# Optimization experiments

Measured on AMD Instinct MI355X. Metric: run time of the kernel, lower is better.

The kernel has to match this reference:

```python
import jax, jax.numpy as jnp
import numpy as np

N = 12  # mmse_block_size
REAL_SIZE = N * (N + 1) // 2  # 78: diag + strict lower
IMAG_SIZE = N * (N - 1) // 2  # 66: strict lower only
ROWS, COLS = jnp.tril_indices(N)        # row-major (i, j<=i) matches torch loop order
ROWS_S, COLS_S = jnp.tril_indices(N, -1)  # strict lower, row-major, matches imag loop
DIAG_MASK = jnp.eye(N, dtype=bool)


def _mlp(x, W1, b1, W2, b2, W3, b3):
    h = jax.nn.relu(x @ W1 + b1)
    h = jax.nn.relu(h @ W2 + b2)
    return h @ W3 + b3


def _cholesky_outer(flat):
    # flat: [B, REAL_SIZE + IMAG_SIZE] -> [B, N, N] complex, L @ L^H
    B = flat.shape[0]
    L_real = jnp.zeros((B, N, N), flat.dtype).at[:, ROWS, COLS].set(flat[:, :REAL_SIZE])
    L_real = jnp.where(DIAG_MASK, jax.nn.softplus(L_real), L_real)
    L_imag = jnp.zeros((B, N, N), flat.dtype).at[:, ROWS_S, COLS_S].set(
        flat[:, REAL_SIZE:REAL_SIZE + IMAG_SIZE])
    L = L_real + 1j * L_imag
    return jnp.einsum('bij,bkj->bik', L, jnp.conj(L))


def setup_inputs() -> dict:
    key = jax.random.key(0)
    ks = jax.random.split(key, 13)
    L, H, OUT = 4096, 64, REAL_SIZE + IMAG_SIZE
    sc = lambda k, shp, fan: (jax.random.normal(k, shp, jnp.float32) / np.sqrt(fan))
    return {
        'channel_stats': jax.random.normal(ks[0], (8192, L), jnp.float32),
        'WC1': sc(ks[1], (L, H), L), 'bC1': jnp.zeros((H,), jnp.float32),
        'WC2': sc(ks[2], (H, H), H), 'bC2': jnp.zeros((H,), jnp.float32),
        'WC3': sc(ks[3], (H, OUT), H), 'bC3': jnp.zeros((OUT,), jnp.float32),
        'WR1': sc(ks[4], (L, H), L), 'bR1': jnp.zeros((H,), jnp.float32),
        'WR2': sc(ks[5], (H, H), H), 'bR2': jnp.zeros((H,), jnp.float32),
        'WR3': sc(ks[6], (H, OUT), H), 'bR3': jnp.zeros((OUT,), jnp.float32),
    }


def reference(channel_stats, WC1, bC1, WC2, bC2, WC3, bC3,
              WR1, bR1, WR2, bR2, WR3, bR3):
    C_flat = _mlp(channel_stats, WC1, bC1, WC2, bC2, WC3, bC3)
    R_flat = _mlp(channel_stats, WR1, bR1, WR2, bR2, WR3, bR3)
    C = _cholesky_outer(C_flat)
    R = _cholesky_outer(R_flat)
    return C, R
```

## Files before the change

kernel.cpp:

```cpp
#include <hip/hip_runtime.h>
#include <stdint.h>

#define M_ROWS 8192
#define K_DIM  4096
#define OUTD   144
#define PLANE  1179648
#define NT     32

typedef __attribute__((ext_vector_type(4))) float  float4v;
typedef __attribute__((ext_vector_type(8))) short  short8v;

static __device__ __forceinline__ unsigned short f2bf(float f) {
    unsigned int u = __builtin_bit_cast(unsigned int, f);
    u += 0x7FFFu + ((u >> 16) & 1u);
    return (unsigned short)(u >> 16);
}

__global__ __launch_bounds__(256) void wt_kernel(
    const float* __restrict__ WC1, const float* __restrict__ WR1,
    unsigned short* __restrict__ Wt) {
    __shared__ float tile[64][65];
    const float* src = (blockIdx.y == 0) ? WC1 : WR1;
    const int k0 = blockIdx.x * 64;
    const int t = threadIdx.x;
    const int j = t & 63, qq = t >> 6;
#pragma unroll
    for (int p = 0; p < 16; ++p) {
        int i = p * 4 + qq;
        tile[i][j] = src[(size_t)(k0 + i) * 64 + j];
    }
    __syncthreads();
    const int tt  = blockIdx.x >> 1;
    const int ksb = (blockIdx.x & 1) * 2;
#pragma unroll
    for (int p = 0; p < 16; ++p) {
        int c = p * 256 + t;
        int e = c & 7, m = (c >> 3) & 15, q = (c >> 7) & 3;
        int ks_l = (c >> 9) & 1, w_l = (c >> 10) & 3;
        int kp = ks_l * 32 + q * 8 + e;
        int np = w_l * 16 + m;
        int wg = blockIdx.y * 4 + w_l;
        size_t dst = ((size_t)(wg * 32 + tt) * 4 + (ksb + ks_l)) * 512
                   + q * 128 + m * 8 + e;
        Wt[dst] = f2bf(tile[kp][np]);
    }
}


#define ISSUE_B(T_, B0_, B1_, B2_, B3_)                          \
    do { const unsigned short* bp_ = bpw + (size_t)(T_) * 2048;  \
         B0_ = *(const short8v*)(bp_ + 0 * 512);                 \
         B1_ = *(const short8v*)(bp_ + 1 * 512);                 \
         B2_ = *(const short8v*)(bp_ + 2 * 512);                 \
         B3_ = *(const short8v*)(bp_ + 3 * 512); } while (0)

#define ISSUE_A(T_, XL_, XH_)                                    \
    do { const float* ap_ = xpw + (size_t)(T_) * 128;            \
         XL_ = *(const float4*)(ap_);                            \
         XH_ = *(const float4*)(ap_ + 4); } while (0)

#define STORE_A(XL_, XH_, BUF_)                                        \
    do { short8v s_;                                                   \
         s_[0] = (short)f2bf((XL_).x); s_[1] = (short)f2bf((XL_).y);   \
         s_[2] = (short)f2bf((XL_).z); s_[3] = (short)f2bf((XL_).w);   \
         s_[4] = (short)f2bf((XH_).x); s_[5] = (short)f2bf((XH_).y);   \
         s_[6] = (short)f2bf((XH_).z); s_[7] = (short)f2bf((XH_).w);   \
         *(short8v*)(Asm_ + (BUF_) * 2048 + (w * 64 + lane) * 8) = s_; } while (0)

#define MFR(BUF_, B0_, B1_, B2_, B3_)                                          \
    do { const unsigned short* ab_ = Asm_ + (BUF_) * 2048 + lane * 8;          \
         short8v a0_ = *(const short8v*)(ab_ + 0 * 512);                       \
         short8v a1_ = *(const short8v*)(ab_ + 1 * 512);                       \
         short8v a2_ = *(const short8v*)(ab_ + 2 * 512);                       \
         short8v a3_ = *(const short8v*)(ab_ + 3 * 512);                       \
         acc = __builtin_amdgcn_mfma_f32_16x16x32_bf16(a0_, B0_, acc, 0, 0, 0);\
         acc = __builtin_amdgcn_mfma_f32_16x16x32_bf16(a1_, B1_, acc, 0, 0, 0);\
         acc = __builtin_amdgcn_mfma_f32_16x16x32_bf16(a2_, B2_, acc, 0, 0, 0);\
         acc = __builtin_amdgcn_mfma_f32_16x16x32_bf16(a3_, B3_, acc, 0, 0, 0);\
    } while (0)

__global__ __launch_bounds__(512, 4) void fused_kernel(
    const float* __restrict__ X, const unsigned short* __restrict__ Wt,
    const float* __restrict__ bC1, const float* __restrict__ bR1,
    const float* __restrict__ WC2, const float* __restrict__ bC2,
    const float* __restrict__ WR2, const float* __restrict__ bR2,
    const float* __restrict__ WC3, const float* __restrict__ bC3,
    const float* __restrict__ WR3, const float* __restrict__ bR3,
    unsigned short* __restrict__ OUT) {
    __shared__ __align__(16) char smem[41216];
    unsigned short* Asm_ = (unsigned short*)smem;
    float* hs  = (float*)smem;
    float* W2s = hs + 16 * 132;
    float* fl  = W2s;

    const int tid  = threadIdx.x;
    const int lane = tid & 63;
    const int w    = tid >> 6;
    const int r0   = blockIdx.x * 16;
    const int m    = lane & 15, q = lane >> 4;

    float4v acc = {0.f, 0.f, 0.f, 0.f};

    const unsigned short* bpw = Wt + (size_t)w * 32 * 2048 + lane * 8;
    const float* xpw = X + (size_t)(r0 + m) * K_DIM + w * 32 + q * 8;
    const bool stager = (w < 4);

    short8v b00, b01, b02, b03, b10, b11, b12, b13;
    float4 xl0, xh0, xl1, xh1;

    ISSUE_B(0, b00, b01, b02, b03);
    if (stager) ISSUE_A(0, xl0, xh0);

#pragma unroll 1
    for (int t = 0; t < NT; t += 2) {
        if (stager) { STORE_A(xl0, xh0, 0); ISSUE_A(t + 1, xl1, xh1); }
        asm volatile("s_waitcnt lgkmcnt(0)" ::: "memory");
        __builtin_amdgcn_s_barrier();
        __builtin_amdgcn_sched_barrier(0);
        ISSUE_B(t + 1, b10, b11, b12, b13);
        MFR(0, b00, b01, b02, b03);
        if (stager) {
            STORE_A(xl1, xh1, 1);
            if (t + 2 < NT) ISSUE_A(t + 2, xl0, xh0);
        }
        asm volatile("s_waitcnt lgkmcnt(0)" ::: "memory");
        __builtin_amdgcn_s_barrier();
        __builtin_amdgcn_sched_barrier(0);
        if (t + 2 < NT) ISSUE_B(t + 2, b00, b01, b02, b03);
        MFR(1, b10, b11, b12, b13);
    }
    __syncthreads();

    {
        const int c = w * 16 + m;
        const float bv = (c < 64) ? bC1[c] : bR1[c - 64];
#pragma unroll
        for (int i = 0; i < 4; ++i) {
            int r = q * 4 + i;
            float v = acc[i] + bv; v = v > 0.f ? v : 0.f;
            hs[r * 132 + c] = v;
        }
    }
#pragma unroll
    for (int p = 0; p < 4; ++p) {
        int fi = p * 512 + tid;
        int k = fi >> 5, c4 = fi & 31;
        int c = c4 * 4;
        const float* wsrc = (c < 64) ? (WC2 + (size_t)k * 64 + c)
                                     : (WR2 + (size_t)k * 64 + (c - 64));
        *(float4*)&W2s[k * 128 + c] = *(const float4*)wsrc;
    }
    __syncthreads();

    const int rg = tid >> 5;
    const int cg = tid & 31;
    const int koff2 = (cg < 16) ? 0 : 64;
    float acc2[4];
    {
        int c = cg * 4;
        const float* bsrc = (c < 64) ? (bC2 + c) : (bR2 + (c - 64));
#pragma unroll
        for (int j = 0; j < 4; ++j) acc2[j] = bsrc[j];
    }
    for (int k = 0; k < 64; ++k) {
        float4 wv = *(const float4*)&W2s[k * 128 + cg * 4];
        float a = hs[rg * 132 + koff2 + k];
        acc2[0] += a * wv.x; acc2[1] += a * wv.y;
        acc2[2] += a * wv.z; acc2[3] += a * wv.w;
    }
    float4 h2v;
    h2v.x = acc2[0] > 0.f ? acc2[0] : 0.f;
    h2v.y = acc2[1] > 0.f ? acc2[1] : 0.f;
    h2v.z = acc2[2] > 0.f ? acc2[2] : 0.f;
    h2v.w = acc2[3] > 0.f ? acc2[3] : 0.f;
    __syncthreads();
    *(float4*)&hs[rg * 132 + cg * 4] = h2v;
    __syncthreads();

#pragma unroll 1
    for (int pass = 0; pass < 3; ++pass) {
        int c = pass * 128 + cg * 4;
        if (c < 288) {
            const int brn = (c >= 144);
            const int cl = c - (brn ? 144 : 0);
            const float* W3 = brn ? WR3 : WC3;
            const float* b3 = brn ? bR3 : bC3;
            const int ko = brn ? 64 : 0;
            float a3[4];
#pragma unroll
            for (int j = 0; j < 4; ++j) a3[j] = b3[cl + j];
            for (int k = 0; k < 64; ++k) {
                float4 wv = *(const float4*)(W3 + (size_t)k * OUTD + cl);
                float a = hs[rg * 132 + ko + k];
                a3[0] += a * wv.x; a3[1] += a * wv.y;
                a3[2] += a * wv.z; a3[3] += a * wv.w;
            }
            float4 v; v.x = a3[0]; v.y = a3[1]; v.z = a3[2]; v.w = a3[3];
            *(float4*)&fl[rg * 288 + c] = v;
        }
    }
    __syncthreads();

    if (tid < 384) {
        int r = tid / 24, rem = tid % 24;
        int brn = rem / 12, ii = rem % 12;
        float* f = &fl[r * 288 + brn * 144];
        int d = ii * (ii + 1) / 2 + ii;
        float xv = f[d];
        f[d] = (xv > 20.f) ? xv : log1pf(expf(xv));
    }
    __syncthreads();

    unsigned int* O32 = (unsigned int*)OUT;
    for (int task = tid; task < 16 * 2 * 78; task += 512) {
        int r = task / 156, rem = task % 156;
        int brn = rem / 78, p = rem % 78;
        int i = 0;
        while (p >= (i + 1) * (i + 2) / 2) ++i;
        int j = p - i * (i + 1) / 2;
        const float* f = &fl[r * 288 + brn * 144];
        const float* g = f + 78;
        const int ti = i * (i + 1) / 2, tj = j * (j + 1) / 2;
        const int si = i * (i - 1) / 2, sj = j * (j - 1) / 2;
        float re = 0.f, im = 0.f;
        for (int k = 0; k <= j; ++k) {
            float ar_ = f[ti + k];
            float ai  = (k == i) ? 0.f : g[si + k];
            float br_ = f[tj + k];
            float bi  = (k == j) ? 0.f : g[sj + k];
            re += ar_ * br_ + ai * bi;
            im += ai * br_ - ar_ * bi;
        }
        unsigned int reb = (unsigned int)f2bf(re);
        unsigned int imb = (unsigned int)f2bf(im);
        unsigned int imn = (unsigned int)f2bf(-im);
        size_t base = brn ? (size_t)PLANE : 0;
        size_t q1 = (size_t)(r0 + r) * 144 + (size_t)(i * 12 + j);
        O32[base + q1] = imb | (reb << 16);
        if (i != j) {
            size_t q2 = (size_t)(r0 + r) * 144 + (size_t)(j * 12 + i);
            O32[base + q2] = imn | (reb << 16);
        }
    }
}

extern "C" void kernel_launch(void* const* d_in, const int* in_sizes, int n_in,
                              void* d_out, int out_size, void* d_ws, size_t ws_size,
                              hipStream_t stream) {
    const float* X   = (const float*)d_in[0];
    const float* WC1 = (const float*)d_in[1];
    const float* bC1 = (const float*)d_in[2];
    const float* WC2 = (const float*)d_in[3];
    const float* bC2 = (const float*)d_in[4];
    const float* WC3 = (const float*)d_in[5];
    const float* bC3 = (const float*)d_in[6];
    const float* WR1 = (const float*)d_in[7];
    const float* bR1 = (const float*)d_in[8];
    const float* WR2 = (const float*)d_in[9];
    const float* bR2 = (const float*)d_in[10];
    const float* WR3 = (const float*)d_in[11];
    const float* bR3 = (const float*)d_in[12];

    unsigned short* Wt = (unsigned short*)d_ws;
    unsigned short* OUT = (unsigned short*)d_out;

    wt_kernel<<<dim3(64, 2), 256, 0, stream>>>(WC1, WR1, Wt);
    fused_kernel<<<M_ROWS / 16, 512, 0, stream>>>(
        X, Wt, bC1, bR1, WC2, bC2, WR2, bR2, WC3, bC3, WR3, bR3, OUT);
}
```

Measured before the change: 261.3 us.

## Stage four K-tiles per barrier with all warps loading A

```diff
diff --git a/kernel.cpp b/kernel.cpp
--- a/kernel.cpp
+++ b/kernel.cpp
@@ -5,7 +5,7 @@
 #define K_DIM  4096
 #define OUTD   144
 #define PLANE  1179648
-#define NT     32
+#define NT2    8
 
 typedef __attribute__((ext_vector_type(4))) float  float4v;
 typedef __attribute__((ext_vector_type(8))) short  short8v;
@@ -47,28 +47,35 @@
 }
 
 
-#define ISSUE_B(T_, B0_, B1_, B2_, B3_)                          \
-    do { const unsigned short* bp_ = bpw + (size_t)(T_) * 2048;  \
+#define ISSUE_B(TB_, B0_, B1_, B2_, B3_)                         \
+    do { const unsigned short* bp_ = bpw + (size_t)(TB_) * 2048; \
          B0_ = *(const short8v*)(bp_ + 0 * 512);                 \
          B1_ = *(const short8v*)(bp_ + 1 * 512);                 \
          B2_ = *(const short8v*)(bp_ + 2 * 512);                 \
          B3_ = *(const short8v*)(bp_ + 3 * 512); } while (0)
 
-#define ISSUE_A(T_, XL_, XH_)                                    \
-    do { const float* ap_ = xpw + (size_t)(T_) * 128;            \
-         XL_ = *(const float4*)(ap_);                            \
-         XH_ = *(const float4*)(ap_ + 4); } while (0)
-
-#define STORE_A(XL_, XH_, BUF_)                                        \
-    do { short8v s_;                                                   \
-         s_[0] = (short)f2bf((XL_).x); s_[1] = (short)f2bf((XL_).y);   \
-         s_[2] = (short)f2bf((XL_).z); s_[3] = (short)f2bf((XL_).w);   \
-         s_[4] = (short)f2bf((XH_).x); s_[5] = (short)f2bf((XH_).y);   \
-         s_[6] = (short)f2bf((XH_).z); s_[7] = (short)f2bf((XH_).w);   \
-         *(short8v*)(Asm_ + (BUF_) * 2048 + (w * 64 + lane) * 8) = s_; } while (0)
-
-#define MFR(BUF_, B0_, B1_, B2_, B3_)                                          \
-    do { const unsigned short* ab_ = Asm_ + (BUF_) * 2048 + lane * 8;          \
+#define ISSUE_A(T_, XA_, XB_, XC_, XD_)                          \
+    do { const float* ap_ = xpw + (size_t)(T_) * 512;            \
+         XA_ = *(const float4*)(ap_);                            \
+         XB_ = *(const float4*)(ap_ + 4);                        \
+         XC_ = *(const float4*)(ap_ + 256);                      \
+         XD_ = *(const float4*)(ap_ + 260); } while (0)
+
+#define STORE_A(BUF_, XA_, XB_, XC_, XD_)                              \
+    do { short8v s1_, s2_;                                             \
+         s1_[0] = (short)f2bf((XA_).x); s1_[1] = (short)f2bf((XA_).y); \
+         s1_[2] = (short)f2bf((XA_).z); s1_[3] = (short)f2bf((XA_).w); \
+         s1_[4] = (short)f2bf((XB_).x); s1_[5] = (short)f2bf((XB_).y); \
+         s1_[6] = (short)f2bf((XB_).z); s1_[7] = (short)f2bf((XB_).w); \
+         s2_[0] = (short)f2bf((XC_).x); s2_[1] = (short)f2bf((XC_).y); \
+         s2_[2] = (short)f2bf((XC_).z); s2_[3] = (short)f2bf((XC_).w); \
+         s2_[4] = (short)f2bf((XD_).x); s2_[5] = (short)f2bf((XD_).y); \
+         s2_[6] = (short)f2bf((XD_).z); s2_[7] = (short)f2bf((XD_).w); \
+         *(short8v*)(Asm_ + (BUF_) * 8192 + (w * 64 + lane) * 8) = s1_; \
+         *(short8v*)(Asm_ + (BUF_) * 8192 + 4096 + (w * 64 + lane) * 8) = s2_; } while (0)
+
+#define MFR(BUF_, SUB_, B0_, B1_, B2_, B3_)                                    \
+    do { const unsigned short* ab_ = Asm_ + (BUF_) * 8192 + (SUB_) * 2048 + lane * 8; \
          short8v a0_ = *(const short8v*)(ab_ + 0 * 512);                       \
          short8v a1_ = *(const short8v*)(ab_ + 1 * 512);                       \
          short8v a2_ = *(const short8v*)(ab_ + 2 * 512);                       \
@@ -103,31 +110,29 @@
 
     const unsigned short* bpw = Wt + (size_t)w * 32 * 2048 + lane * 8;
     const float* xpw = X + (size_t)(r0 + m) * K_DIM + w * 32 + q * 8;
-    const bool stager = (w < 4);
 
     short8v b00, b01, b02, b03, b10, b11, b12, b13;
-    float4 xl0, xh0, xl1, xh1;
-
-    ISSUE_B(0, b00, b01, b02, b03);
-    if (stager) ISSUE_A(0, xl0, xh0);
+    short8v b20, b21, b22, b23, b30, b31, b32, b33;
+    float4 xa0, xa1, xa2, xa3;
+
+    ISSUE_A(0, xa0, xa1, xa2, xa3);
 
 #pragma unroll 1
-    for (int t = 0; t < NT; t += 2) {
-        if (stager) { STORE_A(xl0, xh0, 0); ISSUE_A(t + 1, xl1, xh1); }
+    for (int t = 0; t < NT2; ++t) {
+        const int buf = t & 1;
+        STORE_A(buf, xa0, xa1, xa2, xa3);
+        if (t + 1 < NT2) ISSUE_A(t + 1, xa0, xa1, xa2, xa3);
         asm volatile("s_waitcnt lgkmcnt(0)" ::: "memory");
         __builtin_amdgcn_s_barrier();
         __builtin_amdgcn_sched_barrier(0);
-        ISSUE_B(t + 1, b10, b11, b12, b13);
-        MFR(0, b00, b01, b02, b03);
-        if (stager) {
-            STORE_A(xl1, xh1, 1);
-            if (t + 2 < NT) ISSUE_A(t + 2, xl0, xh0);
-        }
-        asm volatile("s_waitcnt lgkmcnt(0)" ::: "memory");
-        __builtin_amdgcn_s_barrier();
-        __builtin_amdgcn_sched_barrier(0);
-        if (t + 2 < NT) ISSUE_B(t + 2, b00, b01, b02, b03);
-        MFR(1, b10, b11, b12, b13);
+        ISSUE_B(t * 4 + 0, b00, b01, b02, b03);
+        ISSUE_B(t * 4 + 1, b10, b11, b12, b13);
+        ISSUE_B(t * 4 + 2, b20, b21, b22, b23);
+        ISSUE_B(t * 4 + 3, b30, b31, b32, b33);
+        MFR(buf, 0, b00, b01, b02, b03);
+        MFR(buf, 1, b10, b11, b12, b13);
+        MFR(buf, 2, b20, b21, b22, b23);
+        MFR(buf, 3, b30, b31, b32, b33);
     }
     __syncthreads();
 
```

Result: no change. 262.1 us (+0.3%).
